# Kernel tuning notes

Hardware: AMD Instinct MI355X
Metric: run time of the kernel (lower is better)

## Reference

```python
import jax, jax.numpy as jnp
import numpy as np

B, N, D = 4, 1024, 1024
H, DH = 16, 64
MEM = 16
SCALE = DH ** -0.5
EPS = 1e-6


def setup_inputs() -> dict:
    key = jax.random.key(0)
    ks = jax.random.split(key, 8)
    inner = H * DH
    return {
        "x": jax.random.normal(ks[0], (B, N, D), dtype=jnp.float32),
        "mask": jnp.ones((B, N), dtype=bool),
        "Wq": jax.random.normal(ks[1], (D, inner), dtype=jnp.float32) / np.sqrt(D),
        "Wkv": jax.random.normal(ks[2], (D, 2 * inner), dtype=jnp.float32) / np.sqrt(D),
        "Wo": jax.random.normal(ks[3], (inner, D), dtype=jnp.float32) / np.sqrt(inner),
        "mem_k": jax.random.normal(ks[4], (H, MEM, DH), dtype=jnp.float32),
        "mem_v": jax.random.normal(ks[5], (H, MEM, DH), dtype=jnp.float32),
        "th_pre": jax.random.normal(ks[6], (H, H), dtype=jnp.float32) / np.sqrt(H),
        "th_post": jax.random.normal(ks[7], (H, H), dtype=jnp.float32) / np.sqrt(H),
    }


def _l2norm(t):
    return t * jax.lax.rsqrt(jnp.sum(t * t, axis=-1, keepdims=True) + EPS)


def reference(x, mask, Wq, Wkv, Wo, mem_k, mem_v, th_pre, th_post):
    b, n, _ = x.shape
    # projections: b n (h d) -> b h n d
    q = (x @ Wq).reshape(b, n, H, DH).transpose(0, 2, 1, 3)
    kv = (x @ Wkv).reshape(b, n, 2, H, DH)
    k = kv[:, :, 0].transpose(0, 2, 1, 3)
    v = kv[:, :, 1].transpose(0, 2, 1, 3)
    # qk-norm (l2 normalize along head dim)
    q = _l2norm(q)
    k = _l2norm(k)
    # memory key/values: prepend MEM learned slots
    k = jnp.concatenate([jnp.broadcast_to(mem_k[None], (b, H, MEM, DH)), k], axis=2)
    v = jnp.concatenate([jnp.broadcast_to(mem_v[None], (b, H, MEM, DH)), v], axis=2)
    jk = n + MEM
    dots = jnp.einsum('bhid,bhjd->bhij', q, k) * SCALE
    # talking heads pre-softmax: mix across head dim
    dots = jnp.einsum('bhij,hg->bgij', dots, th_pre)
    # causal mask (mem slots always visible) + key padding mask
    i_pos = jnp.arange(n)[:, None]
    j_pos = jnp.arange(jk)[None, :] - MEM
    causal_ok = j_pos <= i_pos  # [n, jk]
    key_mask = jnp.concatenate([jnp.ones((b, MEM), dtype=bool), mask], axis=1)  # [b, jk]
    full_mask = causal_ok[None, None] & key_mask[:, None, None, :]
    neg = jnp.finfo(dots.dtype).min
    dots = jnp.where(full_mask, dots, neg)
    attn = jax.nn.softmax(dots, axis=-1)
    # talking heads post-softmax
    attn = jnp.einsum('bhij,hg->bgij', attn, th_post)
    out = jnp.einsum('bhij,bhjd->bhid', attn, v)
    out = out.transpose(0, 2, 1, 3).reshape(b, n, H * DH)
    return out @ Wo, attn
```

## Files before the change

### kernel.cpp

```cpp
#include <hip/hip_runtime.h>

#define B_ 4
#define N_ 1024
#define D_ 1024
#define H_ 16
#define DH_ 64
#define MEM_ 16
#define JK_ 1040
#define JKP_ 1056
#define SCALE_ 0.125f
#define EPS_ 1e-6f
#define BHN_ 65536
#define SP_ 1092
#define LOG2E_ 1.4426950408889634f

typedef short bf16x8 __attribute__((ext_vector_type(8)));
typedef float f32x4 __attribute__((ext_vector_type(4)));
typedef _Float16 f16x4 __attribute__((ext_vector_type(4)));
typedef _Float16 f16x8 __attribute__((ext_vector_type(8)));
typedef ushort u16x8 __attribute__((ext_vector_type(8)));

union F16x8u { f16x4 h[2]; f16x8 v; };

__device__ __forceinline__ ushort f2b(float f) {
    unsigned u = __builtin_bit_cast(unsigned, f);
    unsigned r = (u + 0x7fffu + ((u >> 16) & 1u)) >> 16;
    return (ushort)r;
}

__device__ __forceinline__ void gload16(const ushort* g, ushort* l) {
    __builtin_amdgcn_global_load_lds((__attribute__((address_space(1))) void*)g,
                                     (__attribute__((address_space(3))) void*)l, 16, 0, 0);
}

__device__ __forceinline__ void snake(int blk, int& b, int& pair, int& strip) {
    int q = blk >> 8, c = blk & 255;
    b = c & 3;
    int r = c >> 2;
    pair = r & 31;
    strip = ((r >> 5) << 1) | q;
}

__global__ void k_cast_x(const float* __restrict__ x, ushort* __restrict__ xb, int n4) {
    int i = blockIdx.x * blockDim.x + threadIdx.x;
    if (i >= n4) return;
    float4 v = ((const float4*)x)[i];
    ushort4 o;
    o.x = f2b(v.x); o.y = f2b(v.y); o.z = f2b(v.z); o.w = f2b(v.w);
    ((ushort4*)xb)[i] = o;
}

__global__ void k_tcast(const float* __restrict__ src, ushort* __restrict__ dst, int R, int C) {
    __shared__ float t[32][33];
    int bx = blockIdx.x * 32, by = blockIdx.y * 32;
    int x = bx + threadIdx.x;
    for (int k = 0; k < 32; k += 8) {
        int y = by + threadIdx.y + k;
        t[threadIdx.y + k][threadIdx.x] = src[(size_t)y * C + x];
    }
    __syncthreads();
    int xo = by + threadIdx.x;
    for (int k = 0; k < 32; k += 8) {
        int yo = bx + threadIdx.y + k;
        dst[(size_t)yo * R + xo] = f2b(t[threadIdx.x][threadIdx.y + k]);
    }
}

__global__ __launch_bounds__(256) void k_gemm(const ushort* __restrict__ A, const ushort* __restrict__ BT,
                                              float* __restrict__ C, int ldc) {
    __shared__ ushort lA[4096];
    __shared__ ushort lB[4096];
    int tid = threadIdx.x, w = tid >> 6, lane = tid & 63;
    int l16 = lane & 15, quad = lane >> 4;
    int wr = w >> 1, wc = w & 1;
    int m0 = blockIdx.y * 128, n0 = blockIdx.x * 128;
    f32x4 acc[4][4];
#pragma unroll
    for (int mi = 0; mi < 4; mi++)
#pragma unroll
        for (int ni = 0; ni < 4; ni++) acc[mi][ni] = (f32x4){0.f, 0.f, 0.f, 0.f};

    int srow = (lane >> 2);
    int cg = lane & 3;
    for (int k0 = 0; k0 < 1024; k0 += 32) {
#pragma unroll
        for (int i = 0; i < 2; i++) {
            int row = w * 32 + i * 16 + srow;
            int cgS = cg ^ ((row >> 1) & 3);
            gload16(A + (size_t)(m0 + row) * 1024 + k0 + cgS * 8, lA + w * 1024 + i * 512);
            gload16(BT + (size_t)(n0 + row) * 1024 + k0 + cgS * 8, lB + w * 1024 + i * 512);
        }
        __syncthreads();
        bf16x8 af[4], bfr[4];
#pragma unroll
        for (int mi = 0; mi < 4; mi++) {
            int arow = wr * 64 + mi * 16 + l16;
            af[mi] = *(const bf16x8*)(lA + arow * 32 + (quad ^ ((arow >> 1) & 3)) * 8);
        }
#pragma unroll
        for (int ni = 0; ni < 4; ni++) {
            int brow = wc * 64 + ni * 16 + l16;
            bfr[ni] = *(const bf16x8*)(lB + brow * 32 + (quad ^ ((brow >> 1) & 3)) * 8);
        }
#pragma unroll
        for (int mi = 0; mi < 4; mi++)
#pragma unroll
            for (int ni = 0; ni < 4; ni++)
                acc[mi][ni] = __builtin_amdgcn_mfma_f32_16x16x32_bf16(af[mi], bfr[ni], acc[mi][ni], 0, 0, 0);
        __syncthreads();
    }
#pragma unroll
    for (int mi = 0; mi < 4; mi++)
#pragma unroll
        for (int ni = 0; ni < 4; ni++)
#pragma unroll
            for (int r = 0; r < 4; r++)
                C[(size_t)(m0 + wr * 64 + mi * 16 + quad * 4 + r) * ldc + n0 + wc * 64 + ni * 16 + l16] =
                    acc[mi][ni][r];
}

__global__ __launch_bounds__(256) void k_norm_qk(const float* __restrict__ proj,
                                                 ushort* __restrict__ qw, ushort* __restrict__ kw) {
    int w = threadIdx.x >> 6, lane = threadIdx.x & 63;
    int id = blockIdx.x * 4 + w;
    int qk = id & 1;
    int h = (id >> 1) & 15;
    int i = (id >> 5) & 1023;
    int b = id >> 15;
    float v = proj[(size_t)(b * N_ + i) * 3072 + qk * 1024 + h * 64 + lane];
    float ss = v * v;
#pragma unroll
    for (int m = 1; m < 64; m <<= 1) ss += __shfl_xor(ss, m);
    float r = rsqrtf(ss + EPS_);
    ushort o = f2b(v * r);
    if (qk == 0)
        qw[((size_t)(b * H_ + h) * N_ + i) * DH_ + lane] = o;
    else
        kw[((size_t)(b * H_ + h) * JKP_ + MEM_ + i) * DH_ + lane] = o;
}

__global__ __launch_bounds__(256) void k_v_transpose(const float* __restrict__ proj, _Float16* __restrict__ vt) {
    __shared__ float t[64][65];
    int bh = blockIdx.x, c = blockIdx.y;
    int b = bh >> 4, h = bh & 15;
    int i0 = c * 64;
#pragma unroll
    for (int l = 0; l < 16; l++) {
        int idx = threadIdx.x + l * 256;
        int il = idx >> 6, d = idx & 63;
        t[il][d] = proj[(size_t)(b * N_ + i0 + il) * 3072 + 2048 + h * 64 + d];
    }
    __syncthreads();
#pragma unroll
    for (int l = 0; l < 16; l++) {
        int idx = threadIdx.x + l * 256;
        int dr = idx >> 6, ic = idx & 63;
        vt[((size_t)(b * H_ + h) * DH_ + dr) * JKP_ + MEM_ + i0 + ic] = (_Float16)t[ic][dr];
    }
}

__global__ void k_mem_fill(const float* __restrict__ mk, const float* __restrict__ mv,
                           ushort* __restrict__ kw, _Float16* __restrict__ vt) {
    int b = blockIdx.x >> 4, h = blockIdx.x & 15;
#pragma unroll
    for (int l = 0; l < 4; l++) {
        int idx = threadIdx.x + l * 256;
        int j = idx >> 6, d = idx & 63;
        kw[((size_t)(b * H_ + h) * JKP_ + j) * DH_ + d] = f2b(mk[(h * MEM_ + j) * DH_ + d]);
        vt[((size_t)(b * H_ + h) * DH_ + d) * JKP_ + j] = (_Float16)mv[(h * MEM_ + j) * DH_ + d];
        kw[((size_t)(b * H_ + h) * JKP_ + JK_ + j) * DH_ + d] = 0;
        vt[((size_t)(b * H_ + h) * DH_ + d) * JKP_ + JK_ + j] = (_Float16)0.f;
    }
}

__global__ void k_zerofill(float* __restrict__ attn) {
    int blk = blockIdx.x;
    int ti = blk & 63, g = (blk >> 6) & 15, b = blk >> 10;
    int zs = 32 * (((ti + 1) >> 1) + 1);
    if (zs >= JK_) return;
    int cols4 = (JK_ - zs) >> 2;
    f32x4 z = (f32x4){0.f, 0.f, 0.f, 0.f};
    for (int r = 0; r < 16; r++) {
        f32x4* base = (f32x4*)(attn + ((size_t)(b * H_ + g) * N_ + ti * 16 + r) * JK_ + zs);
        for (int c4 = threadIdx.x; c4 < cols4; c4 += 256) __builtin_nontemporal_store(z, base + c4);
    }
}


__device__ __forceinline__ void qk_tile(_Float16* ldsD, const ushort* kp,
                                        bf16x8 qa0, bf16x8 qa1, int j0, int h, int l16, int quad) {
#pragma unroll
    for (int js = 0; js < 4; js++) {
        f32x4 d = (f32x4){0.f, 0.f, 0.f, 0.f};
        const ushort* kpp = kp + (size_t)(j0 + js * 16 + l16) * DH_ + quad * 8;
        d = __builtin_amdgcn_mfma_f32_16x16x32_bf16(qa0, *(const bf16x8*)kpp, d, 0, 0, 0);
        d = __builtin_amdgcn_mfma_f32_16x16x32_bf16(qa1, *(const bf16x8*)(kpp + 32), d, 0, 0, 0);
#pragma unroll
        for (int r = 0; r < 4; r++)
            ldsD[h * SP_ + (quad * 4 + r) * 68 + js * 16 + l16] = (_Float16)(d[r] * SCALE_);
    }
}

__device__ __forceinline__ f32x4 premix_frag(const _Float16* ldsD, f16x4 thA,
                                             int row, int jg, int l16, int quad) {
    f16x4 bf;
#pragma unroll
    for (int t = 0; t < 4; t++) bf[t] = ldsD[(quad * 4 + t) * SP_ + row * 68 + jg * 16 + l16];
    return __builtin_amdgcn_mfma_f32_16x16x16f16(thA, bf, (f32x4){0.f, 0.f, 0.f, 0.f}, 0, 0, 0);
}

__global__ __launch_bounds__(512, 6) void k_attn_pass1(
    const ushort* __restrict__ qw, const ushort* __restrict__ kw,
    const float* __restrict__ thpre, float* __restrict__ Sws) {
    __shared__ _Float16 ldsD[16 * SP_];
    int tid = threadIdx.x;
    int w = tid >> 6, lane = tid & 63, l16 = lane & 15, quad = lane >> 4;
    int b, pair, strip;
    snake(blockIdx.x, b, pair, strip);

    f16x4 thA;
#pragma unroll
    for (int t = 0; t < 4; t++) thA[t] = (_Float16)(thpre[(quad * 4 + t) * 16 + l16] * LOG2E_);

    for (int half = 0; half < 2; half++) {
        int ti = half ? (63 - pair) : pair;
        int i0 = ti * 16;
        int Ut = (ti + 1) >> 2;
        int u0 = (strip + ti) & 3;

        bf16x8 qa[2][2];
#pragma unroll
        for (int hi = 0; hi < 2; hi++) {
            int h = w + hi * 8;
            const ushort* qp = qw + ((size_t)(b * H_ + h) * N_ + i0 + l16) * DH_ + quad * 8;
            qa[hi][0] = *(const bf16x8*)(qp);
            qa[hi][1] = *(const bf16x8*)(qp + 32);
        }
        float Ssum[2][4];
#pragma unroll
        for (int rr = 0; rr < 2; rr++)
#pragma unroll
            for (int r = 0; r < 4; r++) Ssum[rr][r] = 0.f;

        for (int u = u0; u <= Ut; u += 4) {
            int j0 = u * 64;
#pragma unroll
            for (int hi = 0; hi < 2; hi++) {
                int h = w + hi * 8;
                qk_tile(ldsD, kw + (size_t)(b * H_ + h) * JKP_ * DH_, qa[hi][0], qa[hi][1], j0, h, l16, quad);
            }
            __syncthreads();
#pragma unroll
            for (int rr = 0; rr < 2; rr++) {
                int row = w + rr * 8;
#pragma unroll
                for (int jg = 0; jg < 4; jg++) {
                    f32x4 L = premix_frag(ldsD, thA, row, jg, l16, quad);
                    int j = j0 + jg * 16 + l16;
                    bool valid = (j - MEM_) <= (i0 + row);
#pragma unroll
                    for (int r = 0; r < 4; r++) Ssum[rr][r] += valid ? exp2f(L[r]) : 0.f;
                }
            }
            __syncthreads();
        }
#pragma unroll
        for (int rr = 0; rr < 2; rr++)
#pragma unroll
            for (int r = 0; r < 4; r++) {
                float s = Ssum[rr][r];
                s += __shfl_xor(s, 1);
                s += __shfl_xor(s, 2);
                s += __shfl_xor(s, 4);
                s += __shfl_xor(s, 8);
                Ssum[rr][r] = s;
            }
        if (l16 == 0) {
#pragma unroll
            for (int rr = 0; rr < 2; rr++)
#pragma unroll
                for (int r = 0; r < 4; r++)
                    Sws[(size_t)strip * BHN_ + (size_t)(b * H_ + quad * 4 + r) * N_ + i0 + w + rr * 8] =
                        Ssum[rr][r];
        }
    }
}

__global__ __launch_bounds__(512, 4) void k_attnmix(
    const ushort* __restrict__ qw, const ushort* __restrict__ kw,
    const float* __restrict__ Sws, const float* __restrict__ thpre,
    const float* __restrict__ thpost, const _Float16* __restrict__ vt,
    float* __restrict__ attn, _Float16* __restrict__ outp) {
    __shared__ _Float16 ldsDP[16 * SP_];
    __shared__ float inv[16][16];
    int tid = threadIdx.x;
    int w = tid >> 6, lane = tid & 63, l16 = lane & 15, quad = lane >> 4;
    int b, pair, strip;
    snake(blockIdx.x, b, pair, strip);

    f16x4 thA, thP;
#pragma unroll
    for (int t = 0; t < 4; t++) {
        thA[t] = (_Float16)(thpre[(quad * 4 + t) * 16 + l16] * LOG2E_);
        thP[t] = (_Float16)thpost[(quad * 4 + t) * 16 + l16];
    }

    for (int half = 0; half < 2; half++) {
        int ti = half ? (63 - pair) : pair;
        int i0 = ti * 16;
        int Ut = (ti + 1) >> 2;
        int u0 = (strip + ti) & 3;

        __syncthreads();
        if (tid < 256) {
            int g = tid >> 4, r = tid & 15;
            size_t base = (size_t)(b * H_ + g) * N_ + i0 + r;
            inv[g][r] = 1.f / (Sws[base] + Sws[(size_t)BHN_ + base] +
                               Sws[2 * (size_t)BHN_ + base] + Sws[3 * (size_t)BHN_ + base]);
        }
        __syncthreads();
        float invr[2][4];
#pragma unroll
        for (int rr = 0; rr < 2; rr++)
#pragma unroll
            for (int r = 0; r < 4; r++) invr[rr][r] = inv[quad * 4 + r][w + rr * 8];

        bf16x8 qa[2][2];
#pragma unroll
        for (int hi = 0; hi < 2; hi++) {
            int h = w + hi * 8;
            const ushort* qp = qw + ((size_t)(b * H_ + h) * N_ + i0 + l16) * DH_ + quad * 8;
            qa[hi][0] = *(const bf16x8*)(qp);
            qa[hi][1] = *(const bf16x8*)(qp + 32);
        }
        f32x4 macc[2][4];
#pragma unroll
        for (int hi = 0; hi < 2; hi++)
#pragma unroll
            for (int dt = 0; dt < 4; dt++) macc[hi][dt] = (f32x4){0.f, 0.f, 0.f, 0.f};

        for (int u = u0; u <= Ut; u += 4) {
            int j0 = u * 64;
#pragma unroll
            for (int hi = 0; hi < 2; hi++) {
                int h = w + hi * 8;
                qk_tile(ldsDP, kw + (size_t)(b * H_ + h) * JKP_ * DH_, qa[hi][0], qa[hi][1], j0, h, l16, quad);
            }
            __syncthreads();
#pragma unroll
            for (int rr = 0; rr < 2; rr++) {
                int row = w + rr * 8;
#pragma unroll
                for (int jg = 0; jg < 4; jg++) {
                    f32x4 L = premix_frag(ldsDP, thA, row, jg, l16, quad);
                    int j = j0 + jg * 16 + l16;
                    bool valid = (j - MEM_) <= (i0 + row);
                    bool jok = j < JK_;
                    f16x4 pf;
#pragma unroll
                    for (int r = 0; r < 4; r++) {
                        float p = valid ? exp2f(L[r]) * invr[rr][r] : 0.f;
                        pf[r] = (_Float16)p;
                    }
                    f32x4 am = __builtin_amdgcn_mfma_f32_16x16x16f16(thP, pf, (f32x4){0.f, 0.f, 0.f, 0.f}, 0, 0, 0);
#pragma unroll
                    for (int r = 0; r < 4; r++) {
                        if (jok)
                            __builtin_nontemporal_store(
                                am[r], &attn[((size_t)(b * H_ + quad * 4 + r) * N_ + i0 + row) * JK_ + j]);
                        ldsDP[(quad * 4 + r) * SP_ + row * 68 + jg * 16 + l16] = (_Float16)am[r];
                    }
                }
            }
            __syncthreads();
#pragma unroll
            for (int hi = 0; hi < 2; hi++) {
                int h = w + hi * 8;
                const _Float16* pb = ldsDP + h * SP_ + l16 * 68 + quad * 8;
                F16x8u pa0, pa1;
                pa0.h[0] = *(const f16x4*)(pb);
                pa0.h[1] = *(const f16x4*)(pb + 4);
                pa1.h[0] = *(const f16x4*)(pb + 32);
                pa1.h[1] = *(const f16x4*)(pb + 36);
                const _Float16* vp = vt + ((size_t)(b * H_ + h) * DH_ + l16) * JKP_ + j0 + quad * 8;
#pragma unroll
                for (int dt = 0; dt < 4; dt++) {
                    macc[hi][dt] = __builtin_amdgcn_mfma_f32_16x16x32_f16(
                        pa0.v, *(const f16x8*)(vp + (size_t)dt * 16 * JKP_), macc[hi][dt], 0, 0, 0);
                    macc[hi][dt] = __builtin_amdgcn_mfma_f32_16x16x32_f16(
                        pa1.v, *(const f16x8*)(vp + (size_t)dt * 16 * JKP_ + 32), macc[hi][dt], 0, 0, 0);
                }
            }
        }
        _Float16* op = outp + (size_t)strip * ((size_t)B_ * H_ * N_ * DH_);
#pragma unroll
        for (int hi = 0; hi < 2; hi++) {
            int h = w + hi * 8;
#pragma unroll
            for (int dt = 0; dt < 4; dt++)
#pragma unroll
                for (int r = 0; r < 4; r++)
                    op[((size_t)(b * H_ + h) * N_ + i0 + quad * 4 + r) * DH_ + dt * 16 + l16] =
                        (_Float16)macc[hi][dt][r];
        }
    }
}

__global__ void k_outcombine(const _Float16* __restrict__ op, ushort* __restrict__ xo) {
    int i8 = blockIdx.x * 256 + threadIdx.x;
    int d8 = i8 & 7, g = (i8 >> 3) & 15, i = (i8 >> 7) & 1023, b = i8 >> 17;
    size_t src8 = ((size_t)(b * H_ + g) * N_ + i) * 8 + d8;
    const size_t STR8 = (size_t)BHN_ * 8;
    f16x8 s0 = ((const f16x8*)op)[src8];
    f16x8 s1 = ((const f16x8*)op)[src8 + STR8];
    f16x8 s2 = ((const f16x8*)op)[src8 + 2 * STR8];
    f16x8 s3 = ((const f16x8*)op)[src8 + 3 * STR8];
    u16x8 o;
#pragma unroll
    for (int k = 0; k < 8; k++) o[k] = f2b((float)s0[k] + (float)s1[k] + (float)s2[k] + (float)s3[k]);
    ((u16x8*)xo)[i8] = o;
}

extern "C" void kernel_launch(void* const* d_in, const int* in_sizes, int n_in,
                              void* d_out, int out_size, void* d_ws, size_t ws_size,
                              hipStream_t stream) {
    const float* x = (const float*)d_in[0];
    const float* Wq = (const float*)d_in[2];
    const float* Wkv = (const float*)d_in[3];
    const float* Wo = (const float*)d_in[4];
    const float* mk = (const float*)d_in[5];
    const float* mv = (const float*)d_in[6];
    const float* thpre = (const float*)d_in[7];
    const float* thpost = (const float*)d_in[8];

    float* out = (float*)d_out;
    float* attn = out + (size_t)B_ * N_ * D_;

    char* ws = (char*)d_ws;
    ushort* WoT = (ushort*)(ws + 0);
    _Float16* vt = (_Float16*)(ws + 2097152);
    ushort* xb = (ushort*)(ws + 10747904);
    float* Sws = (float*)(ws + 10752000);
    ushort* WT = (ushort*)(ws + 19136512);
    ushort* qw = (ushort*)(ws + 25427968);
    ushort* kw = (ushort*)(ws + 33816576);
    float* proj = (float*)(ws + 42467328);
    _Float16* outp = (_Float16*)(ws + 42467328);
    ushort* xo = (ushort*)(ws + 76021760);
    if (ws_size < 92798976) return;

    k_cast_x<<<4096, 256, 0, stream>>>(x, xb, (B_ * N_ * D_) / 4);
    dim3 tb(32, 8);
    k_tcast<<<dim3(32, 32), tb, 0, stream>>>(Wq, WT, 1024, 1024);
    k_tcast<<<dim3(64, 32), tb, 0, stream>>>(Wkv, WT + 1024 * 1024, 1024, 2048);
    k_tcast<<<dim3(32, 32), tb, 0, stream>>>(Wo, WoT, 1024, 1024);
    k_gemm<<<dim3(24, 32), 256, 0, stream>>>(xb, WT, proj, 3072);
    k_norm_qk<<<32768, 256, 0, stream>>>(proj, qw, kw);
    k_v_transpose<<<dim3(64, 16), 256, 0, stream>>>(proj, vt);
    k_mem_fill<<<64, 256, 0, stream>>>(mk, mv, kw, vt);
    k_zerofill<<<4096, 256, 0, stream>>>(attn);
    k_attn_pass1<<<512, 512, 0, stream>>>(qw, kw, thpre, Sws);
    k_attnmix<<<512, 512, 0, stream>>>(qw, kw, Sws, thpre, thpost, vt, attn, outp);
    k_outcombine<<<2048, 256, 0, stream>>>(outp, xo);
    k_gemm<<<dim3(8, 32), 256, 0, stream>>>(xo, WoT, out, 1024);
}
```

Before: 564.3 us.

## Double-buffer score tiles and prefetch K in attention; merge prep kernels

The two attention kernels now keep two LDS planes for the QK score tile and load the next K tile into registers while the current one is mixed. In the mix kernel the next tile's QK MFMAs are issued before the PV MFMAs, so one barrier per iteration can be dropped in pass1. Separately, the cast/transpose prep kernels and the norm/V-transpose/mem-fill kernels are merged into single launches to cut launch overhead. LDS use doubles and pass1's occupancy hint drops from 6 to 4 blocks, which may reduce latency hiding.

Result: no change. 574.6 us (+1.8%).

```diff
diff --git a/kernel.cpp b/kernel.cpp
--- a/kernel.cpp
+++ b/kernel.cpp
@@ -12,6 +12,7 @@
 #define EPS_ 1e-6f
 #define BHN_ 65536
 #define SP_ 1092
+#define PLANESZ_ (16 * SP_)
 #define LOG2E_ 1.4426950408889634f
 
 typedef short bf16x8 __attribute__((ext_vector_type(8)));
@@ -41,29 +42,41 @@
     strip = ((r >> 5) << 1) | q;
 }
 
-__global__ void k_cast_x(const float* __restrict__ x, ushort* __restrict__ xb, int n4) {
-    int i = blockIdx.x * blockDim.x + threadIdx.x;
-    if (i >= n4) return;
-    float4 v = ((const float4*)x)[i];
-    ushort4 o;
-    o.x = f2b(v.x); o.y = f2b(v.y); o.z = f2b(v.z); o.w = f2b(v.w);
-    ((ushort4*)xb)[i] = o;
-}
-
-__global__ void k_tcast(const float* __restrict__ src, ushort* __restrict__ dst, int R, int C) {
+__global__ __launch_bounds__(256) void k_prep(const float* __restrict__ x,
+                                              const float* __restrict__ Wq,
+                                              const float* __restrict__ Wkv,
+                                              const float* __restrict__ Wo,
+                                              ushort* __restrict__ xb, ushort* __restrict__ WT,
+                                              ushort* __restrict__ WoT) {
+    int blk = blockIdx.x, tid = threadIdx.x;
+    if (blk < 4096) {
+        int i = blk * 256 + tid;
+        float4 v = ((const float4*)x)[i];
+        ushort4 o;
+        o.x = f2b(v.x); o.y = f2b(v.y); o.z = f2b(v.z); o.w = f2b(v.w);
+        ((ushort4*)xb)[i] = o;
+        return;
+    }
     __shared__ float t[32][33];
-    int bx = blockIdx.x * 32, by = blockIdx.y * 32;
-    int x = bx + threadIdx.x;
-    for (int k = 0; k < 32; k += 8) {
-        int y = by + threadIdx.y + k;
-        t[threadIdx.y + k][threadIdx.x] = src[(size_t)y * C + x];
-    }
+    const float* src;
+    ushort* dst;
+    int R, C, bx, by;
+    if (blk < 5120) {
+        int r = blk - 4096; src = Wq; dst = WT; R = 1024; C = 1024;
+        bx = (r & 31) * 32; by = (r >> 5) * 32;
+    } else if (blk < 7168) {
+        int r = blk - 5120; src = Wkv; dst = WT + 1024 * 1024; R = 1024; C = 2048;
+        bx = (r & 63) * 32; by = (r >> 6) * 32;
+    } else {
+        int r = blk - 7168; src = Wo; dst = WoT; R = 1024; C = 1024;
+        bx = (r & 31) * 32; by = (r >> 5) * 32;
+    }
+    int tx = tid & 31, ty = tid >> 5;
+    int xx = bx + tx;
+    for (int k = 0; k < 32; k += 8) t[ty + k][tx] = src[(size_t)(by + ty + k) * C + xx];
     __syncthreads();
-    int xo = by + threadIdx.x;
-    for (int k = 0; k < 32; k += 8) {
-        int yo = bx + threadIdx.y + k;
-        dst[(size_t)yo * R + xo] = f2b(t[threadIdx.x][threadIdx.y + k]);
-    }
+    int xo = by + tx;
+    for (int k = 0; k < 32; k += 8) dst[(size_t)(bx + ty + k) * R + xo] = f2b(t[tx][ty + k]);
 }
 
 __global__ __launch_bounds__(256) void k_gemm(const ushort* __restrict__ A, const ushort* __restrict__ BT,
@@ -119,49 +132,53 @@
                     acc[mi][ni][r];
 }
 
-__global__ __launch_bounds__(256) void k_norm_qk(const float* __restrict__ proj,
-                                                 ushort* __restrict__ qw, ushort* __restrict__ kw) {
-    int w = threadIdx.x >> 6, lane = threadIdx.x & 63;
-    int id = blockIdx.x * 4 + w;
-    int qk = id & 1;
-    int h = (id >> 1) & 15;
-    int i = (id >> 5) & 1023;
-    int b = id >> 15;
-    float v = proj[(size_t)(b * N_ + i) * 3072 + qk * 1024 + h * 64 + lane];
-    float ss = v * v;
-#pragma unroll
-    for (int m = 1; m < 64; m <<= 1) ss += __shfl_xor(ss, m);
-    float r = rsqrtf(ss + EPS_);
-    ushort o = f2b(v * r);
-    if (qk == 0)
-        qw[((size_t)(b * H_ + h) * N_ + i) * DH_ + lane] = o;
-    else
-        kw[((size_t)(b * H_ + h) * JKP_ + MEM_ + i) * DH_ + lane] = o;
-}
-
-__global__ __launch_bounds__(256) void k_v_transpose(const float* __restrict__ proj, _Float16* __restrict__ vt) {
-    __shared__ float t[64][65];
-    int bh = blockIdx.x, c = blockIdx.y;
-    int b = bh >> 4, h = bh & 15;
-    int i0 = c * 64;
-#pragma unroll
-    for (int l = 0; l < 16; l++) {
-        int idx = threadIdx.x + l * 256;
-        int il = idx >> 6, d = idx & 63;
-        t[il][d] = proj[(size_t)(b * N_ + i0 + il) * 3072 + 2048 + h * 64 + d];
-    }
-    __syncthreads();
-#pragma unroll
-    for (int l = 0; l < 16; l++) {
-        int idx = threadIdx.x + l * 256;
-        int dr = idx >> 6, ic = idx & 63;
-        vt[((size_t)(b * H_ + h) * DH_ + dr) * JKP_ + MEM_ + i0 + ic] = (_Float16)t[ic][dr];
-    }
-}
-
-__global__ void k_mem_fill(const float* __restrict__ mk, const float* __restrict__ mv,
-                           ushort* __restrict__ kw, _Float16* __restrict__ vt) {
-    int b = blockIdx.x >> 4, h = blockIdx.x & 15;
+__global__ __launch_bounds__(256) void k_qkv(const float* __restrict__ proj,
+                                             const float* __restrict__ mk, const float* __restrict__ mv,
+                                             ushort* __restrict__ qw, ushort* __restrict__ kw,
+                                             _Float16* __restrict__ vt) {
+    int blk = blockIdx.x;
+    if (blk < 32768) {
+        int w = threadIdx.x >> 6, lane = threadIdx.x & 63;
+        int id = blk * 4 + w;
+        int qk = id & 1;
+        int h = (id >> 1) & 15;
+        int i = (id >> 5) & 1023;
+        int b = id >> 15;
+        float v = proj[(size_t)(b * N_ + i) * 3072 + qk * 1024 + h * 64 + lane];
+        float ss = v * v;
+#pragma unroll
+        for (int m = 1; m < 64; m <<= 1) ss += __shfl_xor(ss, m);
+        float r = rsqrtf(ss + EPS_);
+        ushort o = f2b(v * r);
+        if (qk == 0)
+            qw[((size_t)(b * H_ + h) * N_ + i) * DH_ + lane] = o;
+        else
+            kw[((size_t)(b * H_ + h) * JKP_ + MEM_ + i) * DH_ + lane] = o;
+        return;
+    }
+    if (blk < 33792) {
+        __shared__ float t[64][65];
+        int r0 = blk - 32768;
+        int bh = r0 & 63, c = r0 >> 6;
+        int b = bh >> 4, h = bh & 15;
+        int i0 = c * 64;
+#pragma unroll
+        for (int l = 0; l < 16; l++) {
+            int idx = threadIdx.x + l * 256;
+            int il = idx >> 6, d = idx & 63;
+            t[il][d] = proj[(size_t)(b * N_ + i0 + il) * 3072 + 2048 + h * 64 + d];
+        }
+        __syncthreads();
+#pragma unroll
+        for (int l = 0; l < 16; l++) {
+            int idx = threadIdx.x + l * 256;
+            int dr = idx >> 6, ic = idx & 63;
+            vt[((size_t)(b * H_ + h) * DH_ + dr) * JKP_ + MEM_ + i0 + ic] = (_Float16)t[ic][dr];
+        }
+        return;
+    }
+    int r0 = blk - 33792;
+    int b = r0 >> 4, h = r0 & 15;
 #pragma unroll
     for (int l = 0; l < 4; l++) {
         int idx = threadIdx.x + l * 256;
@@ -187,17 +204,68 @@
 }
 
 
-__device__ __forceinline__ void qk_tile(_Float16* ldsD, const ushort* kp,
-                                        bf16x8 qa0, bf16x8 qa1, int j0, int h, int l16, int quad) {
+struct KReg { bf16x8 v[2][4][2]; };
+struct KReg1 { bf16x8 v[4][2]; };
+
+__device__ __forceinline__ void kload2(KReg& kr, const ushort* kwb, int j0, int w, int l16, int quad) {
+#pragma unroll
+    for (int hi = 0; hi < 2; hi++) {
+        const ushort* kp = kwb + (size_t)(w + hi * 8) * (JKP_ * DH_);
+#pragma unroll
+        for (int js = 0; js < 4; js++) {
+            const ushort* kpp = kp + (size_t)(j0 + js * 16 + l16) * DH_ + quad * 8;
+            kr.v[hi][js][0] = *(const bf16x8*)kpp;
+            kr.v[hi][js][1] = *(const bf16x8*)(kpp + 32);
+        }
+    }
+}
+
+__device__ __forceinline__ void kload1(KReg1& kr, const ushort* kp0, int j0, int l16, int quad) {
+#pragma unroll
+    for (int js = 0; js < 4; js++) {
+        const ushort* kpp = kp0 + (size_t)(j0 + js * 16 + l16) * DH_ + quad * 8;
+        kr.v[js][0] = *(const bf16x8*)kpp;
+        kr.v[js][1] = *(const bf16x8*)(kpp + 32);
+    }
+}
+
+__device__ __forceinline__ void amma2(_Float16* buf, const KReg& kr, const bf16x8 (&qa)[2][2],
+                                      int w, int l16, int quad) {
+#pragma unroll
+    for (int hi = 0; hi < 2; hi++) {
+        int h = w + hi * 8;
+#pragma unroll
+        for (int js = 0; js < 4; js++) {
+            f32x4 d = (f32x4){0.f, 0.f, 0.f, 0.f};
+            d = __builtin_amdgcn_mfma_f32_16x16x32_bf16(qa[hi][0], kr.v[hi][js][0], d, 0, 0, 0);
+            d = __builtin_amdgcn_mfma_f32_16x16x32_bf16(qa[hi][1], kr.v[hi][js][1], d, 0, 0, 0);
+#pragma unroll
+            for (int r = 0; r < 4; r++)
+                buf[h * SP_ + (quad * 4 + r) * 68 + js * 16 + l16] = (_Float16)(d[r] * SCALE_);
+        }
+    }
+}
+
+__device__ __forceinline__ void amma1(_Float16* buf, const KReg1& kr, const ushort* kp1,
+                                      const bf16x8 (&qa)[2][2], int w, int l16, int quad, int j0) {
 #pragma unroll
     for (int js = 0; js < 4; js++) {
         f32x4 d = (f32x4){0.f, 0.f, 0.f, 0.f};
-        const ushort* kpp = kp + (size_t)(j0 + js * 16 + l16) * DH_ + quad * 8;
-        d = __builtin_amdgcn_mfma_f32_16x16x32_bf16(qa0, *(const bf16x8*)kpp, d, 0, 0, 0);
-        d = __builtin_amdgcn_mfma_f32_16x16x32_bf16(qa1, *(const bf16x8*)(kpp + 32), d, 0, 0, 0);
+        d = __builtin_amdgcn_mfma_f32_16x16x32_bf16(qa[0][0], kr.v[js][0], d, 0, 0, 0);
+        d = __builtin_amdgcn_mfma_f32_16x16x32_bf16(qa[0][1], kr.v[js][1], d, 0, 0, 0);
 #pragma unroll
         for (int r = 0; r < 4; r++)
-            ldsD[h * SP_ + (quad * 4 + r) * 68 + js * 16 + l16] = (_Float16)(d[r] * SCALE_);
+            buf[w * SP_ + (quad * 4 + r) * 68 + js * 16 + l16] = (_Float16)(d[r] * SCALE_);
+    }
+#pragma unroll
+    for (int js = 0; js < 4; js++) {
+        const ushort* kpp = kp1 + (size_t)(j0 + js * 16 + l16) * DH_ + quad * 8;
+        f32x4 d = (f32x4){0.f, 0.f, 0.f, 0.f};
+        d = __builtin_amdgcn_mfma_f32_16x16x32_bf16(qa[1][0], *(const bf16x8*)kpp, d, 0, 0, 0);
+        d = __builtin_amdgcn_mfma_f32_16x16x32_bf16(qa[1][1], *(const bf16x8*)(kpp + 32), d, 0, 0, 0);
+#pragma unroll
+        for (int r = 0; r < 4; r++)
+            buf[(w + 8) * SP_ + (quad * 4 + r) * 68 + js * 16 + l16] = (_Float16)(d[r] * SCALE_);
     }
 }
 
@@ -209,19 +277,21 @@
     return __builtin_amdgcn_mfma_f32_16x16x16f16(thA, bf, (f32x4){0.f, 0.f, 0.f, 0.f}, 0, 0, 0);
 }
 
-__global__ __launch_bounds__(512, 6) void k_attn_pass1(
+__global__ __launch_bounds__(512, 4) void k_attn_pass1(
     const ushort* __restrict__ qw, const ushort* __restrict__ kw,
     const float* __restrict__ thpre, float* __restrict__ Sws) {
-    __shared__ _Float16 ldsD[16 * SP_];
+    __shared__ _Float16 ldsD[2 * PLANESZ_];
     int tid = threadIdx.x;
     int w = tid >> 6, lane = tid & 63, l16 = lane & 15, quad = lane >> 4;
     int b, pair, strip;
     snake(blockIdx.x, b, pair, strip);
+    const ushort* kwb = kw + (size_t)b * H_ * JKP_ * DH_;
 
     f16x4 thA;
 #pragma unroll
     for (int t = 0; t < 4; t++) thA[t] = (_Float16)(thpre[(quad * 4 + t) * 16 + l16] * LOG2E_);
 
+    int cur = 0;
     for (int half = 0; half < 2; half++) {
         int ti = half ? (63 - pair) : pair;
         int i0 = ti * 16;
@@ -242,27 +312,26 @@
 #pragma unroll
             for (int r = 0; r < 4; r++) Ssum[rr][r] = 0.f;
 
+        KReg kr;
+        kload2(kr, kwb, u0 * 64, w, l16, quad);
         for (int u = u0; u <= Ut; u += 4) {
-            int j0 = u * 64;
-#pragma unroll
-            for (int hi = 0; hi < 2; hi++) {
-                int h = w + hi * 8;
-                qk_tile(ldsD, kw + (size_t)(b * H_ + h) * JKP_ * DH_, qa[hi][0], qa[hi][1], j0, h, l16, quad);
-            }
+            _Float16* buf = ldsD + cur * PLANESZ_;
+            amma2(buf, kr, qa, w, l16, quad);
+            if (u + 4 <= Ut) kload2(kr, kwb, (u + 4) * 64, w, l16, quad);
             __syncthreads();
 #pragma unroll
             for (int rr = 0; rr < 2; rr++) {
                 int row = w + rr * 8;
 #pragma unroll
                 for (int jg = 0; jg < 4; jg++) {
-                    f32x4 L = premix_frag(ldsD, thA, row, jg, l16, quad);
-                    int j = j0 + jg * 16 + l16;
+                    f32x4 L = premix_frag(buf, thA, row, jg, l16, quad);
+                    int j = u * 64 + jg * 16 + l16;
                     bool valid = (j - MEM_) <= (i0 + row);
 #pragma unroll
                     for (int r = 0; r < 4; r++) Ssum[rr][r] += valid ? exp2f(L[r]) : 0.f;
                 }
             }
-            __syncthreads();
+            cur ^= 1;
         }
 #pragma unroll
         for (int rr = 0; rr < 2; rr++)
@@ -283,6 +352,7 @@
                     Sws[(size_t)strip * BHN_ + (size_t)(b * H_ + quad * 4 + r) * N_ + i0 + w + rr * 8] =
                         Ssum[rr][r];
         }
+        __syncthreads();
     }
 }
 
@@ -291,12 +361,13 @@
     const float* __restrict__ Sws, const float* __restrict__ thpre,
     const float* __restrict__ thpost, const _Float16* __restrict__ vt,
     float* __restrict__ attn, _Float16* __restrict__ outp) {
-    __shared__ _Float16 ldsDP[16 * SP_];
+    __shared__ _Float16 ldsDP[2 * PLANESZ_];
     __shared__ float inv[16][16];
     int tid = threadIdx.x;
     int w = tid >> 6, lane = tid & 63, l16 = lane & 15, quad = lane >> 4;
     int b, pair, strip;
     snake(blockIdx.x, b, pair, strip);
+    const ushort* kwb = kw + (size_t)b * H_ * JKP_ * DH_;
 
     f16x4 thA, thP;
 #pragma unroll
@@ -304,6 +375,8 @@
         thA[t] = (_Float16)(thpre[(quad * 4 + t) * 16 + l16] * LOG2E_);
         thP[t] = (_Float16)thpost[(quad * 4 + t) * 16 + l16];
     }
+    const ushort* kp0 = kwb + (size_t)w * (JKP_ * DH_);
+    const ushort* kp1 = kwb + (size_t)(w + 8) * (JKP_ * DH_);
 
     for (int half = 0; half < 2; half++) {
         int ti = half ? (63 - pair) : pair;
@@ -339,20 +412,24 @@
 #pragma unroll
             for (int dt = 0; dt < 4; dt++) macc[hi][dt] = (f32x4){0.f, 0.f, 0.f, 0.f};
 
+        int cur = 0;
+        KReg1 kr;
+        if (u0 <= Ut) {
+            kload1(kr, kp0, u0 * 64, l16, quad);
+            amma1(ldsDP, kr, kp1, qa, w, l16, quad, u0 * 64);
+            if (u0 + 4 <= Ut) kload1(kr, kp0, (u0 + 4) * 64, l16, quad);
+        }
+        __syncthreads();
+
         for (int u = u0; u <= Ut; u += 4) {
+            _Float16* buf = ldsDP + cur * PLANESZ_;
             int j0 = u * 64;
-#pragma unroll
-            for (int hi = 0; hi < 2; hi++) {
-                int h = w + hi * 8;
-                qk_tile(ldsDP, kw + (size_t)(b * H_ + h) * JKP_ * DH_, qa[hi][0], qa[hi][1], j0, h, l16, quad);
-            }
-            __syncthreads();
 #pragma unroll
             for (int rr = 0; rr < 2; rr++) {
                 int row = w + rr * 8;
 #pragma unroll
                 for (int jg = 0; jg < 4; jg++) {
-                    f32x4 L = premix_frag(ldsDP, thA, row, jg, l16, quad);
+                    f32x4 L = premix_frag(buf, thA, row, jg, l16, quad);
                     int j = j0 + jg * 16 + l16;
                     bool valid = (j - MEM_) <= (i0 + row);
                     bool jok = j < JK_;
@@ -368,15 +445,19 @@
                         if (jok)
                             __builtin_nontemporal_store(
                                 am[r], &attn[((size_t)(b * H_ + quad * 4 + r) * N_ + i0 + row) * JK_ + j]);
-                        ldsDP[(quad * 4 + r) * SP_ + row * 68 + jg * 16 + l16] = (_Float16)am[r];
+                        buf[(quad * 4 + r) * SP_ + row * 68 + jg * 16 + l16] = (_Float16)am[r];
                     }
                 }
             }
             __syncthreads();
+            if (u + 4 <= Ut) {
+                amma1(ldsDP + (cur ^ 1) * PLANESZ_, kr, kp1, qa, w, l16, quad, (u + 4) * 64);
+                if (u + 8 <= Ut) kload1(kr, kp0, (u + 8) * 64, l16, quad);
+            }
 #pragma unroll
             for (int hi = 0; hi < 2; hi++) {
                 int h = w + hi * 8;
-                const _Float16* pb = ldsDP + h * SP_ + l16 * 68 + quad * 8;
+                const _Float16* pb = buf + h * SP_ + l16 * 68 + quad * 8;
                 F16x8u pa0, pa1;
                 pa0.h[0] = *(const f16x4*)(pb);
                 pa0.h[1] = *(const f16x4*)(pb + 4);
@@ -391,6 +472,8 @@
                         pa1.v, *(const f16x8*)(vp + (size_t)dt * 16 * JKP_ + 32), macc[hi][dt], 0, 0, 0);
                 }
             }
+            cur ^= 1;
+            __syncthreads();
         }
         _Float16* op = outp + (size_t)strip * ((size_t)B_ * H_ * N_ * DH_);
 #pragma unroll
@@ -449,15 +532,9 @@
     ushort* xo = (ushort*)(ws + 76021760);
     if (ws_size < 92798976) return;
 
-    k_cast_x<<<4096, 256, 0, stream>>>(x, xb, (B_ * N_ * D_) / 4);
-    dim3 tb(32, 8);
-    k_tcast<<<dim3(32, 32), tb, 0, stream>>>(Wq, WT, 1024, 1024);
-    k_tcast<<<dim3(64, 32), tb, 0, stream>>>(Wkv, WT + 1024 * 1024, 1024, 2048);
-    k_tcast<<<dim3(32, 32), tb, 0, stream>>>(Wo, WoT, 1024, 1024);
+    k_prep<<<8192, 256, 0, stream>>>(x, Wq, Wkv, Wo, xb, WT, WoT);
     k_gemm<<<dim3(24, 32), 256, 0, stream>>>(xb, WT, proj, 3072);
-    k_norm_qk<<<32768, 256, 0, stream>>>(proj, qw, kw);
-    k_v_transpose<<<dim3(64, 16), 256, 0, stream>>>(proj, vt);
-    k_mem_fill<<<64, 256, 0, stream>>>(mk, mv, kw, vt);
+    k_qkv<<<33856, 256, 0, stream>>>(proj, mk, mv, qw, kw, vt);
     k_zerofill<<<4096, 256, 0, stream>>>(attn);
     k_attn_pass1<<<512, 512, 0, stream>>>(qw, kw, thpre, Sws);
     k_attnmix<<<512, 512, 0, stream>>>(qw, kw, Sws, thpre, thpost, vt, attn, outp);
```
